# Performance work log

Hardware: AMD Instinct MI355X
Metric: run time of the kernel (lower is better)

Reference implementation:

```python
import jax, jax.numpy as jnp
import numpy as np


def setup_inputs() -> dict:
    key = jax.random.key(0)
    k1, k2, k3, k4 = jax.random.split(key, 4)
    B, S, IN, OUT, ORG = 8, 4096, 1536, 3072, 4
    fan_in_std = (1.0 / IN) ** 0.5
    x = jax.random.normal(k1, (B, S, IN), dtype=jnp.float32)
    weight = jax.random.normal(k2, (ORG, IN, OUT), dtype=jnp.float32) * fan_in_std
    bias = jax.random.normal(k3, (ORG, OUT), dtype=jnp.float32) * 0.01
    organism_index = jax.random.randint(k4, (B,), 0, ORG, dtype=jnp.int64)
    return {"x": x, "organism_index": organism_index, "weight": weight, "bias": bias}


def reference(x, organism_index, weight, bias):
    # Gather per-sample weight [B, IN, OUT] and bias [B, OUT]
    w = weight[organism_index].astype(x.dtype)          # [B, IN, OUT]
    b = bias[organism_index].astype(x.dtype)            # [B, OUT]
    # x: [B, S, IN] -> [B, S, OUT]; bias broadcast over inner dims
    out = jnp.einsum('bsi,bij->bsj', x, w) + b[:, None, :]
    return out
```

## Files before the change

kernel.cpp:

```cpp
#include <hip/hip_runtime.h>
#include <hip/hip_bf16.h>
#include <stdint.h>

typedef __attribute__((ext_vector_type(4)))  float f32x4;
typedef __attribute__((ext_vector_type(16))) float f32x16;
typedef __attribute__((ext_vector_type(8)))  short short8;

#define DIM_S 4096
#define DIM_IN 1536
#define DIM_OUT 3072
#define NB 8
#define NORG 4

#define XB_ELEMS (NB * DIM_S * DIM_IN)
#define WT_ELEMS (NORG * DIM_OUT * DIM_IN)
#define WS_NEED ((size_t)(XB_ELEMS + WT_ELEMS) * 2)
#define NWT_BLOCKS (NORG * 24 * 48)
#define NX_BLOCKS 2048

__device__ __forceinline__ unsigned short f2bf(float f) {
    union { __hip_bfloat16 h; unsigned short u; } c;
    c.h = __float2bfloat16(f);
    return c.u;
}

__device__ __forceinline__ void gload16(const void* g, void* l) {
    __builtin_amdgcn_global_load_lds(
        (const __attribute__((address_space(1))) unsigned int*)g,
        (__attribute__((address_space(3))) unsigned int*)l, 16, 0, 0);
}

__global__ __launch_bounds__(256) void cvt_all(const float* __restrict__ x,
                                               const float* __restrict__ w,
                                               unsigned short* __restrict__ xb,
                                               unsigned short* __restrict__ wt) {
    const int t = threadIdx.x;
    if (blockIdx.x < NWT_BLOCKS) {
        __shared__ unsigned short T[64][68];
        const int bid = blockIdx.x;
        const int org = bid / (24 * 48);
        const int rem = bid % (24 * 48);
        const int k0 = (rem / 48) * 64;
        const int n0 = (rem % 48) * 64;
        const float* __restrict__ wp = w + (size_t)org * DIM_IN * DIM_OUT;
        unsigned short* __restrict__ op = wt + (size_t)org * DIM_OUT * DIM_IN;
        #pragma unroll
        for (int i = 0; i < 4; ++i) {
            const int c = t + 256 * i;
            const int kk = c >> 4, nq = (c & 15) * 4;
            const float4 v = *reinterpret_cast<const float4*>(
                wp + (size_t)(k0 + kk) * DIM_OUT + n0 + nq);
            ushort4 pv;
            pv.x = f2bf(v.x); pv.y = f2bf(v.y); pv.z = f2bf(v.z); pv.w = f2bf(v.w);
            *reinterpret_cast<ushort4*>(&T[kk][nq]) = pv;
        }
        __syncthreads();
        #pragma unroll
        for (int i = 0; i < 2; ++i) {
            const int c = t + 256 * i;
            const int n = c >> 3, k8 = (c & 7) * 8;
            union { unsigned short u[8]; short8 v; } p;
            #pragma unroll
            for (int j = 0; j < 8; ++j) p.u[j] = T[k8 + j][n];
            *reinterpret_cast<short8*>(op + (size_t)(n0 + n) * DIM_IN + k0 + k8) = p.v;
        }
    } else {
        const int nchunk = XB_ELEMS / 8;
        const int xb0 = blockIdx.x - NWT_BLOCKS;
        for (int c = xb0 * 256 + t; c < nchunk; c += NX_BLOCKS * 256) {
            const float4 v0 = *reinterpret_cast<const float4*>(x + (size_t)c * 8);
            const float4 v1 = *reinterpret_cast<const float4*>(x + (size_t)c * 8 + 4);
            union { unsigned short u[8]; short8 v; } p;
            p.u[0] = f2bf(v0.x); p.u[1] = f2bf(v0.y); p.u[2] = f2bf(v0.z); p.u[3] = f2bf(v0.w);
            p.u[4] = f2bf(v1.x); p.u[5] = f2bf(v1.y); p.u[6] = f2bf(v1.z); p.u[7] = f2bf(v1.w);
            *reinterpret_cast<short8*>(xb + (size_t)c * 8) = p.v;
        }
    }
}

__global__ __launch_bounds__(512, 2) void mol_gemm_8p(
    const unsigned short* __restrict__ xb, const int* __restrict__ orgidx,
    const unsigned short* __restrict__ wt, const float* __restrict__ bias,
    float* __restrict__ out)
{
    __shared__ __align__(16) unsigned short LDS[2][4][8192];

    const int tid  = threadIdx.x;
    const int lane = tid & 63;
    const int wave = tid >> 6;
    const int wr = wave >> 2;
    const int wc = wave & 3;
    const int l31 = lane & 31;
    const int lhi = lane >> 5;

    const int bid = blockIdx.x;
    const int id  = (bid & 7) * 192 + (bid >> 3);
    const int row0 = (id / 12) * 256;
    const int col0 = (id % 12) * 256;
    const int org  = orgidx[row0 >> 12];

    const unsigned short* __restrict__ Abase = xb + (size_t)row0 * DIM_IN;
    const unsigned short* __restrict__ Bbase =
        wt + (size_t)org * DIM_OUT * DIM_IN + (size_t)col0 * DIM_IN;

    const int rA = tid >> 2;
    const int sstg = ((((tid >> 5) & 1) << 1) | ((tid >> 6) & 1));
    const int qs = ((tid & 3) ^ sstg) * 8;
    const unsigned short* pA0 = Abase + (size_t)rA * DIM_IN + qs;
    const unsigned short* pA1 = Abase + (size_t)(128 + rA) * DIM_IN + qs;
    const unsigned short* pB0 = Bbase + (size_t)rA * DIM_IN + qs;
    const unsigned short* pB1 = Bbase + (size_t)(128 + rA) * DIM_IN + qs;

    const int d0 = wave * 512;
    const int d1 = 4096 + wave * 512;

    const int swr = ((((l31 >> 3) & 1) << 1) | ((l31 >> 4) & 1));
    const int cks0 = (lhi ^ (swr & 1)) + 2 * ((swr >> 1) & 1);
    const unsigned ldsbase = (unsigned)(unsigned long long)
        (const __attribute__((address_space(3))) unsigned short*)&LDS[0][0][0];
    const unsigned rbA = ldsbase + (unsigned)((wr * 128 + l31) * 64);
    const unsigned rbB = ldsbase + (unsigned)((wc * 64  + l31) * 64);
    const unsigned adrA_ks0 = rbA + (unsigned)(cks0 * 16);
    const unsigned adrA_ks1 = rbA + (unsigned)((cks0 ^ 2) * 16);
    const unsigned adrB_ks0 = rbB + (unsigned)(cks0 * 16);
    const unsigned adrB_ks1 = rbB + (unsigned)((cks0 ^ 2) * 16);

    f32x16 acc[4][2] = {};
    short8 af[2][4], bfr[2][4];

#define STG(buf, slot, p0, p1, kofs) do {                      \
        gload16((p0) + (kofs), &LDS[buf][slot][d0]);           \
        gload16((p1) + (kofs), &LDS[buf][slot][d1]);           \
    } while (0)

#define DSR(dst, addr, imm)                                                 \
    asm volatile("ds_read_b128 %0, %1 offset:%c2"                           \
                 : "=v"(dst) : "v"(addr), "i"(imm))

#define RD_A4(dst, buf, kk, mih) do {                                       \
        const unsigned o0_ = adrA_ks0 + (buf) * 65536u + (kk) * 16384u;     \
        const unsigned o1_ = adrA_ks1 + (buf) * 65536u + (kk) * 16384u;     \
        DSR(af[dst][0], o0_, ((mih)*2 + 0) * 2048);                         \
        DSR(af[dst][1], o1_, ((mih)*2 + 0) * 2048);                         \
        DSR(af[dst][2], o0_, ((mih)*2 + 1) * 2048);                         \
        DSR(af[dst][3], o1_, ((mih)*2 + 1) * 2048);                         \
    } while (0)

#define RD_B4(dst, buf, kk) do {                                            \
        const unsigned o0_ = adrB_ks0 + (buf) * 65536u + (2+(kk)) * 16384u; \
        const unsigned o1_ = adrB_ks1 + (buf) * 65536u + (2+(kk)) * 16384u; \
        DSR(bfr[dst][0], o0_, 0);                                           \
        DSR(bfr[dst][1], o1_, 0);                                           \
        DSR(bfr[dst][2], o0_, 2048);                                        \
        DSR(bfr[dst][3], o1_, 2048);                                        \
    } while (0)

#define MM(ca, cb, mih) do {                                                \
        __builtin_amdgcn_s_setprio(1);                                      \
        _Pragma("unroll")                                                   \
        for (int ml_ = 0; ml_ < 2; ++ml_) {                                 \
            _Pragma("unroll")                                               \
            for (int nf_ = 0; nf_ < 2; ++nf_) {                             \
                acc[(mih)*2 + ml_][nf_] =                                   \
                    __builtin_amdgcn_mfma_f32_32x32x16_bf16(                \
                        af[ca][ml_*2 + 0], bfr[cb][nf_*2 + 0],              \
                        acc[(mih)*2 + ml_][nf_], 0, 0, 0);                  \
                acc[(mih)*2 + ml_][nf_] =                                   \
                    __builtin_amdgcn_mfma_f32_32x32x16_bf16(                \
                        af[ca][ml_*2 + 1], bfr[cb][nf_*2 + 1],              \
                        acc[(mih)*2 + ml_][nf_], 0, 0, 0);                  \
            }                                                               \
        }                                                                   \
        __builtin_amdgcn_s_setprio(0);                                      \
    } while (0)

#define BAR  do { __builtin_amdgcn_s_barrier();                             \
                  asm volatile("" ::: "memory"); } while (0)
#define WAIT4 asm volatile("s_waitcnt vmcnt(4)" ::: "memory")
#define WAIT8 asm volatile("s_waitcnt vmcnt(8)" ::: "memory")
#define WAITL(n) do { asm volatile("s_waitcnt lgkmcnt(" #n ")");            \
                      __builtin_amdgcn_sched_barrier(0); } while (0)
#define KADV(k) do { if ((k) < 1504) (k) += 32; } while (0)

    STG(0, 0, pA0, pA1, 0);
    STG(0, 2, pB0, pB1, 0);
    STG(0, 1, pA0, pA1, 32);
    STG(0, 3, pB0, pB1, 32);
    STG(1, 0, pA0, pA1, 64);
    STG(1, 2, pB0, pB1, 64);
    WAIT8;
    BAR;
    RD_A4(0, 0, 0, 0);
    RD_B4(0, 0, 0);

    int kA = 96, kB = 96;

#define TILE2() do {                                                          \
   STG(1,1,pA0,pA1,kA); KADV(kA); RD_A4(1, 0,0,1);                      \
         WAITL(4); MM(0,0,0);                 BAR;                            \
   STG(1,3,pB0,pB1,kB); KADV(kB); RD_A4(0, 0,1,0); RD_B4(1, 0,1);      \
         WAITL(8); MM(1,0,1);          WAIT4; BAR;                            \
   STG(0,0,pA0,pA1,kA); KADV(kA); RD_A4(1, 0,1,1);                      \
         WAITL(4); MM(0,1,0);                 BAR;                            \
   STG(0,2,pB0,pB1,kB); KADV(kB); RD_A4(0, 1,0,0); RD_B4(0, 1,0);      \
         WAITL(8); MM(1,1,1);          WAIT4; BAR;                            \
   STG(0,1,pA0,pA1,kA); KADV(kA); RD_A4(1, 1,0,1);                      \
         WAITL(4); MM(0,0,0);                 BAR;                            \
   STG(0,3,pB0,pB1,kB); KADV(kB); RD_A4(0, 1,1,0); RD_B4(1, 1,1);      \
         WAITL(8); MM(1,0,1);          WAIT4; BAR;                            \
   STG(1,0,pA0,pA1,kA); KADV(kA); RD_A4(1, 1,1,1);                      \
         WAITL(4); MM(0,1,0);                 BAR;                            \
   STG(1,2,pB0,pB1,kB); KADV(kB); RD_A4(0, 0,0,0); RD_B4(0, 0,0);      \
         WAITL(8); MM(1,1,1);          WAIT4; BAR;                            \
} while (0)

    #pragma unroll 1
    for (int i = 0; i < 12; ++i) {
        TILE2();
    }

    asm volatile("s_waitcnt lgkmcnt(0)");

    const float* __restrict__ bptr = bias + (size_t)org * DIM_OUT;
    #pragma unroll
    for (int nf = 0; nf < 2; ++nf) {
        const int gc = col0 + wc * 64 + nf * 32 + l31;
        const float bv = bptr[gc];
        #pragma unroll
        for (int mf = 0; mf < 4; ++mf) {
            const int grb = row0 + wr * 128 + mf * 32 + 4 * lhi;
            #pragma unroll
            for (int reg = 0; reg < 16; ++reg) {
                const int gr = grb + (reg & 3) + 8 * (reg >> 2);
                out[(size_t)gr * DIM_OUT + gc] = acc[mf][nf][reg] + bv;
            }
        }
    }
#undef STG
#undef DSR
#undef RD_A4
#undef RD_B4
#undef MM
#undef BAR
#undef WAIT4
#undef WAIT8
#undef WAITL
#undef KADV
#undef TILE2
}

#define BM 128
#define BN 128
#define BK 32
#define LDK 40
union BF8 { unsigned short u[8]; short8 v; };

__global__ __launch_bounds__(256) void mol_gemm_fb(
    const float* __restrict__ x, const int* __restrict__ orgidx,
    const float* __restrict__ weight, const float* __restrict__ bias,
    float* __restrict__ out)
{
    __shared__ __align__(16) unsigned short Alds[2][BM][LDK];
    __shared__ __align__(16) unsigned short Blds[2][BN][LDK];

    const int tid  = threadIdx.x;
    const int lane = tid & 63;
    const int wave = tid >> 6;
    const int wr = wave >> 1, wc = wave & 1;

    const int bid = blockIdx.x;
    const int id  = (bid & 7) * 768 + (bid >> 3);
    const int row0 = (id / 24) * BM;
    const int col0 = (id % 24) * BN;

    const int batch = row0 / DIM_S;
    const int org   = orgidx[batch];
    const float* __restrict__ W = weight + (size_t)org * DIM_IN * DIM_OUT;

    f32x4 acc[4][4] = {};
    const int ar  = tid >> 2;
    const int ak8 = (tid & 3) * 8;
    const int bn  = tid & 127;
    const int bg0 = tid >> 7;
    const float* __restrict__ xbase = x + (size_t)row0 * DIM_IN;
    const float* __restrict__ wbase = W + col0 + bn;

    auto stage = [&](int buf, int k0) {
        #pragma unroll
        for (int i = 0; i < 2; ++i) {
            const int r = ar + 64 * i;
            const float* xp = xbase + (size_t)r * DIM_IN + k0 + ak8;
            const float4 v0 = *reinterpret_cast<const float4*>(xp);
            const float4 v1 = *reinterpret_cast<const float4*>(xp + 4);
            BF8 p;
            p.u[0] = f2bf(v0.x); p.u[1] = f2bf(v0.y);
            p.u[2] = f2bf(v0.z); p.u[3] = f2bf(v0.w);
            p.u[4] = f2bf(v1.x); p.u[5] = f2bf(v1.y);
            p.u[6] = f2bf(v1.z); p.u[7] = f2bf(v1.w);
            *reinterpret_cast<short8*>(&Alds[buf][r][ak8]) = p.v;
        }
        #pragma unroll
        for (int j = 0; j < 2; ++j) {
            const int g = bg0 + 2 * j;
            const float* wp = wbase + (size_t)(k0 + 8 * g) * DIM_OUT;
            BF8 p;
            #pragma unroll
            for (int r = 0; r < 8; ++r) p.u[r] = f2bf(wp[(size_t)r * DIM_OUT]);
            *reinterpret_cast<short8*>(&Blds[buf][bn][8 * g]) = p.v;
        }
    };

    stage(0, 0);
    const int nk = DIM_IN / BK;
    const int kq = (lane >> 4) * 8;
    const int lr = lane & 15;

    for (int t = 0; t < nk; ++t) {
        __syncthreads();
        const int cur = t & 1;
        if (t + 1 < nk) stage(cur ^ 1, (t + 1) * BK);
        short8 a[4], b[4];
        #pragma unroll
        for (int mi = 0; mi < 4; ++mi)
            a[mi] = *reinterpret_cast<const short8*>(&Alds[cur][wr * 64 + mi * 16 + lr][kq]);
        #pragma unroll
        for (int ni = 0; ni < 4; ++ni)
            b[ni] = *reinterpret_cast<const short8*>(&Blds[cur][wc * 64 + ni * 16 + lr][kq]);
        #pragma unroll
        for (int mi = 0; mi < 4; ++mi)
            #pragma unroll
            for (int ni = 0; ni < 4; ++ni)
                acc[mi][ni] = __builtin_amdgcn_mfma_f32_16x16x32_bf16(
                    a[mi], b[ni], acc[mi][ni], 0, 0, 0);
    }

    const float* __restrict__ bptr = bias + (size_t)org * DIM_OUT;
    const int crow = (lane >> 4) * 4;
    const int ccol = lane & 15;
    #pragma unroll
    for (int ni = 0; ni < 4; ++ni) {
        const int gc = col0 + wc * 64 + ni * 16 + ccol;
        const float bv = bptr[gc];
        #pragma unroll
        for (int mi = 0; mi < 4; ++mi) {
            const int gr = row0 + wr * 64 + mi * 16 + crow;
            #pragma unroll
            for (int r = 0; r < 4; ++r)
                out[(size_t)(gr + r) * DIM_OUT + gc] = acc[mi][ni][r] + bv;
        }
    }
}

extern "C" void kernel_launch(void* const* d_in, const int* in_sizes, int n_in,
                              void* d_out, int out_size, void* d_ws, size_t ws_size,
                              hipStream_t stream)
{
    const float* x      = (const float*)d_in[0];
    const int*   orgidx = (const int*)d_in[1];
    const float* weight = (const float*)d_in[2];
    const float* bias   = (const float*)d_in[3];
    float* out = (float*)d_out;

    if (ws_size >= WS_NEED) {
        unsigned short* xbp = (unsigned short*)d_ws;
        unsigned short* wtp = xbp + XB_ELEMS;
        cvt_all<<<dim3(NWT_BLOCKS + NX_BLOCKS), dim3(256), 0, stream>>>(
            x, weight, xbp, wtp);
        mol_gemm_8p<<<dim3(1536), dim3(512), 0, stream>>>(xbp, orgidx, wtp, bias, out);
    } else {
        mol_gemm_fb<<<dim3(6144), dim3(256), 0, stream>>>(x, orgidx, weight, bias, out);
    }
}
```

Baseline: 401.3 us.

## Remove LDS fragment double-buffering; read fragments then wait before each MFMA block

```diff
diff --git a/kernel.cpp b/kernel.cpp
--- a/kernel.cpp
+++ b/kernel.cpp
@@ -126,7 +126,7 @@
     const unsigned adrB_ks1 = rbB + (unsigned)((cks0 ^ 2) * 16);
 
     f32x16 acc[4][2] = {};
-    short8 af[2][4], bfr[2][4];
+    short8 af4[4], bfr[4];
 
 #define STG(buf, slot, p0, p1, kofs) do {                      \
         gload16((p0) + (kofs), &LDS[buf][slot][d0]);           \
@@ -137,25 +137,25 @@
     asm volatile("ds_read_b128 %0, %1 offset:%c2"                           \
                  : "=v"(dst) : "v"(addr), "i"(imm))
 
-#define RD_A4(dst, buf, kk, mih) do {                                       \
+#define RD_A4(buf, kk, mih) do {                                            \
         const unsigned o0_ = adrA_ks0 + (buf) * 65536u + (kk) * 16384u;     \
         const unsigned o1_ = adrA_ks1 + (buf) * 65536u + (kk) * 16384u;     \
-        DSR(af[dst][0], o0_, ((mih)*2 + 0) * 2048);                         \
-        DSR(af[dst][1], o1_, ((mih)*2 + 0) * 2048);                         \
-        DSR(af[dst][2], o0_, ((mih)*2 + 1) * 2048);                         \
-        DSR(af[dst][3], o1_, ((mih)*2 + 1) * 2048);                         \
+        DSR(af4[0], o0_, ((mih)*2 + 0) * 2048);                             \
+        DSR(af4[1], o1_, ((mih)*2 + 0) * 2048);                             \
+        DSR(af4[2], o0_, ((mih)*2 + 1) * 2048);                             \
+        DSR(af4[3], o1_, ((mih)*2 + 1) * 2048);                             \
     } while (0)
 
-#define RD_B4(dst, buf, kk) do {                                            \
+#define RD_B4(buf, kk) do {                                                 \
         const unsigned o0_ = adrB_ks0 + (buf) * 65536u + (2+(kk)) * 16384u; \
         const unsigned o1_ = adrB_ks1 + (buf) * 65536u + (2+(kk)) * 16384u; \
-        DSR(bfr[dst][0], o0_, 0);                                           \
-        DSR(bfr[dst][1], o1_, 0);                                           \
-        DSR(bfr[dst][2], o0_, 2048);                                        \
-        DSR(bfr[dst][3], o1_, 2048);                                        \
+        DSR(bfr[0], o0_, 0);                                                \
+        DSR(bfr[1], o1_, 0);                                                \
+        DSR(bfr[2], o0_, 2048);                                             \
+        DSR(bfr[3], o1_, 2048);                                             \
     } while (0)
 
-#define MM(ca, cb, mih) do {                                                \
+#define MM(mih) do {                                                        \
         __builtin_amdgcn_s_setprio(1);                                      \
         _Pragma("unroll")                                                   \
         for (int ml_ = 0; ml_ < 2; ++ml_) {                                 \
@@ -163,11 +163,11 @@
             for (int nf_ = 0; nf_ < 2; ++nf_) {                             \
                 acc[(mih)*2 + ml_][nf_] =                                   \
                     __builtin_amdgcn_mfma_f32_32x32x16_bf16(                \
-                        af[ca][ml_*2 + 0], bfr[cb][nf_*2 + 0],              \
+                        af4[ml_*2 + 0], bfr[nf_*2 + 0],                     \
                         acc[(mih)*2 + ml_][nf_], 0, 0, 0);                  \
                 acc[(mih)*2 + ml_][nf_] =                                   \
                     __builtin_amdgcn_mfma_f32_32x32x16_bf16(                \
-                        af[ca][ml_*2 + 1], bfr[cb][nf_*2 + 1],              \
+                        af4[ml_*2 + 1], bfr[nf_*2 + 1],                     \
                         acc[(mih)*2 + ml_][nf_], 0, 0, 0);                  \
             }                                                               \
         }                                                                   \
@@ -178,8 +178,8 @@
                   asm volatile("" ::: "memory"); } while (0)
 #define WAIT4 asm volatile("s_waitcnt vmcnt(4)" ::: "memory")
 #define WAIT8 asm volatile("s_waitcnt vmcnt(8)" ::: "memory")
-#define WAITL(n) do { asm volatile("s_waitcnt lgkmcnt(" #n ")");            \
-                      __builtin_amdgcn_sched_barrier(0); } while (0)
+#define WAITL0 do { asm volatile("s_waitcnt lgkmcnt(0)");                   \
+                    __builtin_amdgcn_sched_barrier(0); } while (0)
 #define KADV(k) do { if ((k) < 1504) (k) += 32; } while (0)
 
     STG(0, 0, pA0, pA1, 0);
@@ -190,28 +190,26 @@
     STG(1, 2, pB0, pB1, 64);
     WAIT8;
     BAR;
-    RD_A4(0, 0, 0, 0);
-    RD_B4(0, 0, 0);
 
     int kA = 96, kB = 96;
 
 #define TILE2() do {                                                          \
-   STG(1,1,pA0,pA1,kA); KADV(kA); RD_A4(1, 0,0,1);                      \
-         WAITL(4); MM(0,0,0);                 BAR;                            \
-   STG(1,3,pB0,pB1,kB); KADV(kB); RD_A4(0, 0,1,0); RD_B4(1, 0,1);      \
-         WAITL(8); MM(1,0,1);          WAIT4; BAR;                            \
-   STG(0,0,pA0,pA1,kA); KADV(kA); RD_A4(1, 0,1,1);                      \
-         WAITL(4); MM(0,1,0);                 BAR;                            \
-   STG(0,2,pB0,pB1,kB); KADV(kB); RD_A4(0, 1,0,0); RD_B4(0, 1,0);      \
-         WAITL(8); MM(1,1,1);          WAIT4; BAR;                            \
-   STG(0,1,pA0,pA1,kA); KADV(kA); RD_A4(1, 1,0,1);                      \
-         WAITL(4); MM(0,0,0);                 BAR;                            \
-   STG(0,3,pB0,pB1,kB); KADV(kB); RD_A4(0, 1,1,0); RD_B4(1, 1,1);      \
-         WAITL(8); MM(1,0,1);          WAIT4; BAR;                            \
-   STG(1,0,pA0,pA1,kA); KADV(kA); RD_A4(1, 1,1,1);                      \
-         WAITL(4); MM(0,1,0);                 BAR;                            \
-   STG(1,2,pB0,pB1,kB); KADV(kB); RD_A4(0, 0,0,0); RD_B4(0, 0,0);      \
-         WAITL(8); MM(1,1,1);          WAIT4; BAR;                            \
+   RD_A4(0,0,0); RD_B4(0,0); STG(1,1,pA0,pA1,kA); KADV(kA);             \
+         BAR; WAITL0; MM(0);                 BAR;                             \
+   RD_A4(0,0,1);             STG(1,3,pB0,pB1,kB); KADV(kB);             \
+         BAR; WAITL0; MM(1);          WAIT4; BAR;                             \
+   RD_A4(0,1,0); RD_B4(0,1); STG(0,0,pA0,pA1,kA); KADV(kA);             \
+         BAR; WAITL0; MM(0);                 BAR;                             \
+   RD_A4(0,1,1);             STG(0,2,pB0,pB1,kB); KADV(kB);             \
+         BAR; WAITL0; MM(1);          WAIT4; BAR;                             \
+   RD_A4(1,0,0); RD_B4(1,0); STG(0,1,pA0,pA1,kA); KADV(kA);             \
+         BAR; WAITL0; MM(0);                 BAR;                             \
+   RD_A4(1,0,1);             STG(0,3,pB0,pB1,kB); KADV(kB);             \
+         BAR; WAITL0; MM(1);          WAIT4; BAR;                             \
+   RD_A4(1,1,0); RD_B4(1,1); STG(1,0,pA0,pA1,kA); KADV(kA);             \
+         BAR; WAITL0; MM(0);                 BAR;                             \
+   RD_A4(1,1,1);             STG(1,2,pB0,pB1,kB); KADV(kB);             \
+         BAR; WAITL0; MM(1);          WAIT4; BAR;                             \
 } while (0)
 
     #pragma unroll 1
@@ -244,7 +242,7 @@
 #undef BAR
 #undef WAIT4
 #undef WAIT8
-#undef WAITL
+#undef WAITL0
 #undef KADV
 #undef TILE2
 }
```

After: 407.0 us. Within noise of the previous version (+1.4%).
